# Kernel optimization log

Hardware: AMD Instinct MI355X
Metric: run time of the kernel (lower is better)

## Reference

```python
import jax, jax.numpy as jnp
import numpy as np


def _rx(state, theta, axis):
    # Apply RX(theta) to qubit at tensor axis `axis`. state: (B, 2,...,2) complex.
    half = theta * 0.5
    c = jnp.cos(half)
    s = jnp.sin(half)
    a0 = jnp.take(state, 0, axis=axis)
    a1 = jnp.take(state, 1, axis=axis)
    return jnp.stack([c * a0 - 1j * s * a1, c * a1 - 1j * s * a0], axis=axis)


def _cnot(state, w):
    # CNOT with control wire w (axis w+1), target wire w+1 (axis w+2).
    c_ax = w + 1
    s0 = jnp.take(state, 0, axis=c_ax)
    # after removing the control axis, the target axis index becomes c_ax
    s1 = jnp.flip(jnp.take(state, 1, axis=c_ax), axis=c_ax)
    return jnp.stack([s0, s1], axis=c_ax)


def _run_circuit(x, params):
    # x: (B, n) encoding angles; params: (depth, n) trainable RX angles.
    B, n = x.shape
    depth = params.shape[0]
    state = jnp.zeros((B,) + (2,) * n, jnp.complex64)
    state = state.at[(slice(None),) + (0,) * n].set(1.0 + 0.0j)
    # angle encoding: RX(x_w) on each wire
    for w in range(n):
        theta = x[:, w].reshape((B,) + (1,) * (n - 1))
        state = _rx(state, theta, w + 1)
    # variational layers: RX(param) per wire, then CNOT chain
    for d in range(depth):
        for w in range(n):
            state = _rx(state, params[d, w], w + 1)
        for w in range(n - 1):
            state = _cnot(state, w)
    probs = state.real ** 2 + state.imag ** 2  # (B, 2,...,2)
    ez = []
    for w in range(n):
        axes = tuple(a for a in range(1, n + 1) if a != w + 1)
        p = probs.sum(axes)  # (B, 2)
        ez.append(p[:, 0] - p[:, 1])  # <Z_w>
    return jnp.stack(ez, axis=1)  # (B, n)


def setup_inputs() -> dict:
    key = jax.random.key(0)
    k0, k1, k2, k3, k4 = jax.random.split(key, 5)
    seq_len, batch, input_dim = 256, 128, 64
    n_qubits, depth, hidden = 10, 2, 256
    inputs = jax.random.normal(k0, (seq_len, batch, input_dim), jnp.float32)
    mask = jax.random.randint(k1, (seq_len, batch), 0, 2).astype(jnp.int32)
    qparams = jax.random.normal(k2, (4, depth, n_qubits), jnp.float32)
    W = jax.random.normal(k3, (4, hidden, n_qubits), jnp.float32) / np.sqrt(n_qubits)
    b = jax.random.normal(k4, (4, hidden), jnp.float32) * 0.01
    return {"inputs": inputs, "mask": mask, "qparams": qparams, "W": W, "b": b}


def reference(inputs, mask, qparams, W, b):
    seq_len, batch, _ = inputs.shape
    n = qparams.shape[-1]
    hidden = W.shape[1]
    maskf = mask.astype(inputs.dtype)

    circuits4 = jax.vmap(_run_circuit, in_axes=(None, 0))  # over the 4 gates

    def step(carry, xm):
        hx, cx = carry
        x_t, m_t = xm
        q_in = jnp.concatenate([x_t, hx], axis=1)[:, :n]  # (B, n)
        z = circuits4(q_in, qparams)                      # (4, B, n)
        pre = jnp.einsum('gbn,ghn->gbh', z, W) + b[:, None, :]
        f = jax.nn.sigmoid(pre[0])
        i = jax.nn.sigmoid(pre[1])
        g = jnp.tanh(pre[2])
        o = jax.nn.sigmoid(pre[3])
        m = m_t[:, None]
        f = f * m + (1.0 - m)
        i = i * m
        g = g * m
        o = o * m + (1.0 - m)
        cx_new = f * cx + i * g
        hx_new = o * jnp.tanh(cx_new)
        return (hx_new, cx_new), hx_new

    h0 = jnp.zeros((batch, hidden), inputs.dtype)
    c0 = jnp.zeros((batch, hidden), inputs.dtype)
    (hx, cx), outputs = jax.lax.scan(jax.checkpoint(step), (h0, c0), (inputs, maskf))
    return outputs, (hx, cx)
```

## Files before the change

kernel.cpp:

```cpp
#include <hip/hip_runtime.h>

#define T_LEN 256
#define BATCH 128
#define NQ 10
#define HID 256
#define OUT_HX (T_LEN * BATCH * HID)
#define OUT_CX (OUT_HX + BATCH * HID)
#define ZSTRIDE 40
#define ZROW 44
#define TROW 65

#define KS  (-1.44269504089f)
#define KT2 (-2.88539008178f)

__global__ __launch_bounds__(256) void zker(
    const float* __restrict__ inputs,
    const float* __restrict__ qparams,
    float* __restrict__ zws)
{
  const int b   = blockIdx.x;
  const int tq  = blockIdx.y;
  const int tid = threadIdx.x;
  const int t   = tq * 64 + (tid >> 2);
  const int g   = tid & 3;

  const float sg = (g == 2) ? KT2 : KS;

  float th0[NQ], cth[NQ], sth[NQ];
#pragma unroll
  for (int k = 0; k < NQ; ++k) {
    th0[k]   = qparams[g * 2 * NQ + k];
    float t1 = qparams[g * 2 * NQ + NQ + k];
    sth[k] = __sinf(t1);
    cth[k] = __cosf(t1);
  }
  float cphi[NQ], sphi[NQ];
  const float* xp = inputs + (t * BATCH + b) * 64;
#pragma unroll
  for (int k = 0; k < NQ; ++k) {
    float ang = xp[k] + th0[k];
    sphi[k] = __sinf(ang);
    cphi[k] = __cosf(ang);
  }
  float* zout = zws + (b * T_LEN + t) * ZSTRIDE + g;
#pragma unroll
  for (int w = 0; w < NQ; ++w) {
    float vI, vZ, vY, vX; int js;
    if (w == NQ - 1) { vI = 0.f; vZ = cth[NQ-1]; vY = sth[NQ-1]; vX = 0.f; js = NQ - 2; }
    else             { vI = 1.f; vZ = 0.f; vY = 0.f; vX = 0.f; js = w; }
#pragma unroll
    for (int j = js; j >= 0; --j) {
      float nI = cth[j] * (cphi[j+1] * vZ - sphi[j+1] * vY);
      float nZ = cth[j] * vI;
      float nY = sth[j] * vX;
      float nX = -sth[j] * (sphi[j+1] * vZ + cphi[j+1] * vY);
      vI = nI; vZ = nZ; vY = nY; vX = nX;
    }
    zout[w * 4] = (vI + cphi[0] * vZ - sphi[0] * vY) * sg;
  }
}

__global__ __launch_bounds__(512) void scanker(
    const float* __restrict__ zws,
    const int*  __restrict__ mask,
    const float* __restrict__ W,
    const float* __restrict__ bias,
    float* __restrict__ out)
{
  const int b    = blockIdx.x;
  const int h0   = blockIdx.y * 64;
  const int tid  = threadIdx.x;
  const int lane = tid & 63;
  const int wavu = __builtin_amdgcn_readfirstlane(tid >> 6);

  __shared__ float zlds[T_LEN * ZROW];
  __shared__ float tlds[64 * TROW];
  __shared__ float mk[T_LEN];

  {
    const float4* zg = (const float4*)(zws + b * T_LEN * ZSTRIDE);
    for (int i = tid; i < T_LEN * 10; i += 512) {
      int t = i / 10, c4 = i - t * 10;
      *(float4*)&zlds[t * ZROW + c4 * 4] = zg[i];
    }
  }
  for (int t = tid; t < T_LEN; t += 512) mk[t] = (float)mask[t * BATCH + b];
  __syncthreads();

  float carry[8];
#pragma unroll
  for (int i = 0; i < 8; ++i) carry[i] = 0.f;

  for (int r = 0; r < 4; ++r) {
    const int t = r * 64 + lane;
    float4 z4[10];
#pragma unroll
    for (int n = 0; n < NQ; ++n) z4[n] = *(const float4*)&zlds[t * ZROW + n * 4];
    const float m = mk[t];
    const float onem = 1.f - m;

#pragma unroll
    for (int hh = 0; hh < 8; ++hh) {
      const int h = h0 + wavu * 8 + hh;
      const int wb = __builtin_amdgcn_readfirstlane(h * NQ);

      float p0 = bias[0 * HID + h] * KS;
      float p1 = bias[1 * HID + h] * KS;
      float p2 = bias[2 * HID + h] * KT2;
      float p3 = bias[3 * HID + h] * KS;
#pragma unroll
      for (int n = 0; n < NQ; ++n) {
        p0 = fmaf(z4[n].x, W[0 * HID * NQ + wb + n], p0);
        p1 = fmaf(z4[n].y, W[1 * HID * NQ + wb + n], p1);
        p2 = fmaf(z4[n].z, W[2 * HID * NQ + wb + n], p2);
        p3 = fmaf(z4[n].w, W[3 * HID * NQ + wb + n], p3);
      }
      const float uf = __builtin_amdgcn_rcpf(1.f + __builtin_amdgcn_exp2f(p0));
      const float ui = __builtin_amdgcn_rcpf(1.f + __builtin_amdgcn_exp2f(p1));
      const float ug = __builtin_amdgcn_rcpf(1.f + __builtin_amdgcn_exp2f(p2));
      const float uo = __builtin_amdgcn_rcpf(1.f + __builtin_amdgcn_exp2f(p3));

      const float fm = fmaf(m, uf, onem);
      const float gb = fmaf(2.f, ug, -1.f);
      float wt = m * ui * gb;
      const float om = fmaf(m, uo, onem);

      float a = fm, wv = wt;
#pragma unroll
      for (int d = 1; d < 64; d <<= 1) {
        float au = __shfl_up(a, d, 64);
        float wu = __shfl_up(wv, d, 64);
        const bool p = (lane >= d);
        au = p ? au : 1.f;
        wu = p ? wu : 0.f;
        wv = fmaf(a, wu, wv);
        a  = a * au;
      }
      const float ct = fmaf(a, carry[hh], wv);
      carry[hh] = __shfl(ct, 63, 64);

      const float ec = __builtin_amdgcn_exp2f(ct * KT2);
      const float tc = fmaf(2.f, __builtin_amdgcn_rcpf(1.f + ec), -1.f);
      const float hv = om * tc;

      tlds[lane * TROW + wavu * 8 + hh] = hv;

      if (r == 3 && lane == 63) {
        out[OUT_HX + b * HID + h] = hv;
        out[OUT_CX + b * HID + h] = ct;
      }
    }
    __syncthreads();
#pragma unroll
    for (int s = 0; s < 2; ++s) {
      const int q = tid + s * 512;
      const int tt = q >> 4, c = q & 15;
      float4 v;
      v.x = tlds[tt * TROW + 4 * c + 0];
      v.y = tlds[tt * TROW + 4 * c + 1];
      v.z = tlds[tt * TROW + 4 * c + 2];
      v.w = tlds[tt * TROW + 4 * c + 3];
      *(float4*)&out[(r * 64 + tt) * (BATCH * HID) + b * HID + h0 + 4 * c] = v;
    }
    __syncthreads();
  }
}

extern "C" void kernel_launch(void* const* d_in, const int* in_sizes, int n_in,
                              void* d_out, int out_size, void* d_ws, size_t ws_size,
                              hipStream_t stream)
{
  int ii = 0, im = 1, iq = 2, iw = 3, ib = 4;
  for (int i = 0; i < n_in; ++i) {
    switch (in_sizes[i]) {
      case 2097152: ii = i; break;
      case 32768:   im = i; break;
      case 80:      iq = i; break;
      case 10240:   iw = i; break;
      case 1024:    ib = i; break;
      default: break;
    }
  }
  const float* inputs  = (const float*)d_in[ii];
  const int*   mask    = (const int*)d_in[im];
  const float* qparams = (const float*)d_in[iq];
  const float* W       = (const float*)d_in[iw];
  const float* bias    = (const float*)d_in[ib];
  float*       out     = (float*)d_out;
  float*       zws     = (float*)d_ws;

  zker<<<dim3(BATCH, 4), dim3(256), 0, stream>>>(inputs, qparams, zws);
  scanker<<<dim3(BATCH, 4), dim3(512), 0, stream>>>(zws, mask, W, bias, out);
}
```

Before: 108.3 us.

## Interleave gate math with wave scans and double-buffer output staging

Changes the z workspace layout to qubit-major float4 rows so LDS loads are contiguous per timestep. Hoists the bias loads out of the time loop and precomputes the bpermute source indices. Interleaves the gate evaluation of four hidden units with the scan levels of four others, using ds_bpermute, to hide the cross-lane latency. Double-buffers the transpose staging buffer so the trailing barrier can be dropped. The cost is more live registers, which may hurt occupancy at 512 threads.

New measurement: 108.8 us. About the same (+0.5%).

```diff
diff --git a/kernel.cpp b/kernel.cpp
--- a/kernel.cpp
+++ b/kernel.cpp
@@ -6,8 +6,6 @@
 #define HID 256
 #define OUT_HX (T_LEN * BATCH * HID)
 #define OUT_CX (OUT_HX + BATCH * HID)
-#define ZSTRIDE 40
-#define ZROW 44
 #define TROW 65
 
 #define KS  (-1.44269504089f)
@@ -42,7 +40,7 @@
     sphi[k] = __sinf(ang);
     cphi[k] = __cosf(ang);
   }
-  float* zout = zws + (b * T_LEN + t) * ZSTRIDE + g;
+  float* zout = zws + (b * NQ * T_LEN + t) * 4 + g;
 #pragma unroll
   for (int w = 0; w < NQ; ++w) {
     float vI, vZ, vY, vX; int js;
@@ -56,9 +54,61 @@
       float nX = -sth[j] * (sphi[j+1] * vZ + cphi[j+1] * vY);
       vI = nI; vZ = nZ; vY = nY; vX = nX;
     }
-    zout[w * 4] = (vI + cphi[0] * vZ - sphi[0] * vY) * sg;
+    zout[w * T_LEN * 4] = (vI + cphi[0] * vZ - sphi[0] * vY) * sg;
   }
 }
+
+
+#define GATEBODY(HH)                                                     \
+  {                                                                      \
+    const int h_ = h0 + wavu * 8 + (HH);                                 \
+    const int wb_ = __builtin_amdgcn_readfirstlane(h_ * NQ);             \
+    float p0 = bsc[HH][0], p1 = bsc[HH][1], p2 = bsc[HH][2], p3 = bsc[HH][3]; \
+    _Pragma("unroll")                                                    \
+    for (int n = 0; n < NQ; ++n) {                                       \
+      p0 = fmaf(z4[n].x, W[0 * HID * NQ + wb_ + n], p0);                 \
+      p1 = fmaf(z4[n].y, W[1 * HID * NQ + wb_ + n], p1);                 \
+      p2 = fmaf(z4[n].z, W[2 * HID * NQ + wb_ + n], p2);                 \
+      p3 = fmaf(z4[n].w, W[3 * HID * NQ + wb_ + n], p3);                 \
+    }                                                                    \
+    const float uf = __builtin_amdgcn_rcpf(1.f + __builtin_amdgcn_exp2f(p0)); \
+    const float ui = __builtin_amdgcn_rcpf(1.f + __builtin_amdgcn_exp2f(p1)); \
+    const float ug = __builtin_amdgcn_rcpf(1.f + __builtin_amdgcn_exp2f(p2)); \
+    const float uo = __builtin_amdgcn_rcpf(1.f + __builtin_amdgcn_exp2f(p3)); \
+    a8[HH]  = fmaf(m, uf, onem);                                         \
+    w8[HH]  = m * ui * fmaf(2.f, ug, -1.f);                              \
+    om8[HH] = fmaf(m, uo, onem);                                         \
+  }
+
+#define BP(SRC, V) __int_as_float(__builtin_amdgcn_ds_bpermute((SRC), __float_as_int(V)))
+
+#define SCANLEV1(K, HH)                                                  \
+  {                                                                      \
+    float au = BP(srcA[K], a8[HH]);                                      \
+    float wu = BP(srcA[K], w8[HH]);                                      \
+    au = pm[K] ? au : 1.f;                                               \
+    wu = pm[K] ? wu : 0.f;                                               \
+    w8[HH] = fmaf(a8[HH], wu, w8[HH]);                                   \
+    a8[HH] = a8[HH] * au;                                                \
+  }
+
+#define SCANLEV4(K, H0, H1, H2, H3)                                      \
+  SCANLEV1(K, H0) SCANLEV1(K, H1) SCANLEV1(K, H2) SCANLEV1(K, H3)
+
+#define CPHASE(HH)                                                       \
+  {                                                                      \
+    const float ct = fmaf(a8[HH], carry[HH], w8[HH]);                    \
+    carry[HH] = __shfl(ct, 63, 64);                                      \
+    const float ec = __builtin_amdgcn_exp2f(ct * KT2);                   \
+    const float tc = fmaf(2.f, __builtin_amdgcn_rcpf(1.f + ec), -1.f);   \
+    const float hv = om8[HH] * tc;                                       \
+    tlds[p][lane * TROW + wavu * 8 + (HH)] = hv;                         \
+    if (r == 3 && lane == 63) {                                          \
+      const int h_ = h0 + wavu * 8 + (HH);                               \
+      out[OUT_HX + b * HID + h_] = hv;                                   \
+      out[OUT_CX + b * HID + h_] = ct;                                   \
+    }                                                                    \
+  }
 
 __global__ __launch_bounds__(512) void scanker(
     const float* __restrict__ zws,
@@ -73,96 +123,77 @@
   const int lane = tid & 63;
   const int wavu = __builtin_amdgcn_readfirstlane(tid >> 6);
 
-  __shared__ float zlds[T_LEN * ZROW];
-  __shared__ float tlds[64 * TROW];
-  __shared__ float mk[T_LEN];
+  __shared__ float4 zl4[NQ * T_LEN];
+  __shared__ float  tlds[2][64 * TROW];
+  __shared__ float  mk[T_LEN];
 
   {
-    const float4* zg = (const float4*)(zws + b * T_LEN * ZSTRIDE);
-    for (int i = tid; i < T_LEN * 10; i += 512) {
-      int t = i / 10, c4 = i - t * 10;
-      *(float4*)&zlds[t * ZROW + c4 * 4] = zg[i];
-    }
+    const float4* zg = (const float4*)(zws + b * NQ * T_LEN * 4);
+    for (int i = tid; i < NQ * T_LEN; i += 512) zl4[i] = zg[i];
   }
   for (int t = tid; t < T_LEN; t += 512) mk[t] = (float)mask[t * BATCH + b];
   __syncthreads();
 
+  int srcA[6]; bool pm[6];
+#pragma unroll
+  for (int k = 0; k < 6; ++k) {
+    const int d = 1 << k;
+    pm[k]   = (lane >= d);
+    srcA[k] = ((lane >= d) ? (lane - d) : lane) << 2;
+  }
+
+  float bsc[8][4];
+#pragma unroll
+  for (int hh = 0; hh < 8; ++hh) {
+    const int h = h0 + wavu * 8 + hh;
+    bsc[hh][0] = bias[0 * HID + h] * KS;
+    bsc[hh][1] = bias[1 * HID + h] * KS;
+    bsc[hh][2] = bias[2 * HID + h] * KT2;
+    bsc[hh][3] = bias[3 * HID + h] * KS;
+  }
+
   float carry[8];
 #pragma unroll
   for (int i = 0; i < 8; ++i) carry[i] = 0.f;
 
   for (int r = 0; r < 4; ++r) {
+    const int p = r & 1;
     const int t = r * 64 + lane;
-    float4 z4[10];
-#pragma unroll
-    for (int n = 0; n < NQ; ++n) z4[n] = *(const float4*)&zlds[t * ZROW + n * 4];
+    float4 z4[NQ];
+#pragma unroll
+    for (int n = 0; n < NQ; ++n) z4[n] = zl4[n * T_LEN + t];
     const float m = mk[t];
     const float onem = 1.f - m;
 
-#pragma unroll
-    for (int hh = 0; hh < 8; ++hh) {
-      const int h = h0 + wavu * 8 + hh;
-      const int wb = __builtin_amdgcn_readfirstlane(h * NQ);
-
-      float p0 = bias[0 * HID + h] * KS;
-      float p1 = bias[1 * HID + h] * KS;
-      float p2 = bias[2 * HID + h] * KT2;
-      float p3 = bias[3 * HID + h] * KS;
-#pragma unroll
-      for (int n = 0; n < NQ; ++n) {
-        p0 = fmaf(z4[n].x, W[0 * HID * NQ + wb + n], p0);
-        p1 = fmaf(z4[n].y, W[1 * HID * NQ + wb + n], p1);
-        p2 = fmaf(z4[n].z, W[2 * HID * NQ + wb + n], p2);
-        p3 = fmaf(z4[n].w, W[3 * HID * NQ + wb + n], p3);
-      }
-      const float uf = __builtin_amdgcn_rcpf(1.f + __builtin_amdgcn_exp2f(p0));
-      const float ui = __builtin_amdgcn_rcpf(1.f + __builtin_amdgcn_exp2f(p1));
-      const float ug = __builtin_amdgcn_rcpf(1.f + __builtin_amdgcn_exp2f(p2));
-      const float uo = __builtin_amdgcn_rcpf(1.f + __builtin_amdgcn_exp2f(p3));
-
-      const float fm = fmaf(m, uf, onem);
-      const float gb = fmaf(2.f, ug, -1.f);
-      float wt = m * ui * gb;
-      const float om = fmaf(m, uo, onem);
-
-      float a = fm, wv = wt;
-#pragma unroll
-      for (int d = 1; d < 64; d <<= 1) {
-        float au = __shfl_up(a, d, 64);
-        float wu = __shfl_up(wv, d, 64);
-        const bool p = (lane >= d);
-        au = p ? au : 1.f;
-        wu = p ? wu : 0.f;
-        wv = fmaf(a, wu, wv);
-        a  = a * au;
-      }
-      const float ct = fmaf(a, carry[hh], wv);
-      carry[hh] = __shfl(ct, 63, 64);
-
-      const float ec = __builtin_amdgcn_exp2f(ct * KT2);
-      const float tc = fmaf(2.f, __builtin_amdgcn_rcpf(1.f + ec), -1.f);
-      const float hv = om * tc;
-
-      tlds[lane * TROW + wavu * 8 + hh] = hv;
-
-      if (r == 3 && lane == 63) {
-        out[OUT_HX + b * HID + h] = hv;
-        out[OUT_CX + b * HID + h] = ct;
-      }
-    }
+    float a8[8], w8[8], om8[8];
+
+    GATEBODY(0) GATEBODY(1) GATEBODY(2) GATEBODY(3)
+    SCANLEV4(0, 0, 1, 2, 3) GATEBODY(4)
+    SCANLEV4(1, 0, 1, 2, 3) GATEBODY(5)
+    SCANLEV4(2, 0, 1, 2, 3) GATEBODY(6)
+    SCANLEV4(3, 0, 1, 2, 3) GATEBODY(7)
+    SCANLEV4(4, 0, 1, 2, 3)
+    SCANLEV4(5, 0, 1, 2, 3)
+    SCANLEV4(0, 4, 5, 6, 7) CPHASE(0)
+    SCANLEV4(1, 4, 5, 6, 7) CPHASE(1)
+    SCANLEV4(2, 4, 5, 6, 7) CPHASE(2)
+    SCANLEV4(3, 4, 5, 6, 7) CPHASE(3)
+    SCANLEV4(4, 4, 5, 6, 7)
+    SCANLEV4(5, 4, 5, 6, 7)
+    CPHASE(4) CPHASE(5) CPHASE(6) CPHASE(7)
+
     __syncthreads();
 #pragma unroll
     for (int s = 0; s < 2; ++s) {
       const int q = tid + s * 512;
       const int tt = q >> 4, c = q & 15;
       float4 v;
-      v.x = tlds[tt * TROW + 4 * c + 0];
-      v.y = tlds[tt * TROW + 4 * c + 1];
-      v.z = tlds[tt * TROW + 4 * c + 2];
-      v.w = tlds[tt * TROW + 4 * c + 3];
+      v.x = tlds[p][tt * TROW + 4 * c + 0];
+      v.y = tlds[p][tt * TROW + 4 * c + 1];
+      v.z = tlds[p][tt * TROW + 4 * c + 2];
+      v.w = tlds[p][tt * TROW + 4 * c + 3];
       *(float4*)&out[(r * 64 + tt) * (BATCH * HID) + b * HID + h0 + 4 * c] = v;
     }
-    __syncthreads();
   }
 }
 
```

## Restructure scan kernel: hidden units on lanes, chunked time scan across waves

Applied to the files above, without the earlier changes.

Rewrites the scan kernel so each lane owns one hidden unit with its W rows kept in registers, and each wave processes a 32-step time chunk sequentially. Chunk summaries (A, Wc) are combined through LDS, then each wave recomputes its chunk with the correct carry-in and writes outputs directly with coalesced stores across lanes. This removes the 64-lane shuffle scans, the LDS staging of z and of the output transpose, and the per-element W loads. In exchange the gate preactivations are computed twice and z rows are read from global memory as wave-uniform loads. It also adds an occupancy hint to launch bounds.

New measurement: 111.8 us. 3.2% more time.

```diff
diff --git a/kernel.cpp b/kernel.cpp
--- a/kernel.cpp
+++ b/kernel.cpp
@@ -6,9 +6,6 @@
 #define HID 256
 #define OUT_HX (T_LEN * BATCH * HID)
 #define OUT_CX (OUT_HX + BATCH * HID)
-#define ZSTRIDE 40
-#define ZROW 44
-#define TROW 65
 
 #define KS  (-1.44269504089f)
 #define KT2 (-2.88539008178f)
@@ -42,7 +39,7 @@
     sphi[k] = __sinf(ang);
     cphi[k] = __cosf(ang);
   }
-  float* zout = zws + (b * T_LEN + t) * ZSTRIDE + g;
+  float* zout = zws + (b * T_LEN + t) * 40 + g;
 #pragma unroll
   for (int w = 0; w < NQ; ++w) {
     float vI, vZ, vY, vX; int js;
@@ -60,7 +57,7 @@
   }
 }
 
-__global__ __launch_bounds__(512) void scanker(
+__global__ __launch_bounds__(512, 4) void scanker(
     const float* __restrict__ zws,
     const int*  __restrict__ mask,
     const float* __restrict__ W,
@@ -72,97 +69,95 @@
   const int tid  = threadIdx.x;
   const int lane = tid & 63;
   const int wavu = __builtin_amdgcn_readfirstlane(tid >> 6);
+  const int h    = h0 + lane;
 
-  __shared__ float zlds[T_LEN * ZROW];
-  __shared__ float tlds[64 * TROW];
   __shared__ float mk[T_LEN];
+  __shared__ float cA[8][64];
+  __shared__ float cW[8][64];
 
-  {
-    const float4* zg = (const float4*)(zws + b * T_LEN * ZSTRIDE);
-    for (int i = tid; i < T_LEN * 10; i += 512) {
-      int t = i / 10, c4 = i - t * 10;
-      *(float4*)&zlds[t * ZROW + c4 * 4] = zg[i];
-    }
+  for (int t = tid; t < T_LEN; t += 512) mk[t] = (float)mask[t * BATCH + b];
+
+  float Wf[NQ], Wi[NQ], Wg[NQ], Wo[NQ];
+#pragma unroll
+  for (int n = 0; n < NQ; ++n) {
+    Wf[n] = W[(0 * HID + h) * NQ + n];
+    Wi[n] = W[(1 * HID + h) * NQ + n];
+    Wg[n] = W[(2 * HID + h) * NQ + n];
+    Wo[n] = W[(3 * HID + h) * NQ + n];
   }
-  for (int t = tid; t < T_LEN; t += 512) mk[t] = (float)mask[t * BATCH + b];
+  const float bf = bias[0 * HID + h] * KS;
+  const float bi = bias[1 * HID + h] * KS;
+  const float bg = bias[2 * HID + h] * KT2;
+  const float bo = bias[3 * HID + h] * KS;
+
+  const float* zb = zws + b * T_LEN * 40;
   __syncthreads();
 
-  float carry[8];
+  float A = 1.f, Wc = 0.f;
+  for (int k = 0; k < 32; ++k) {
+    const int t = wavu * 32 + k;
+    const float4* zrow = (const float4*)(zb + t * 40);
+    float4 z4[NQ];
 #pragma unroll
-  for (int i = 0; i < 8; ++i) carry[i] = 0.f;
-
-  for (int r = 0; r < 4; ++r) {
-    const int t = r * 64 + lane;
-    float4 z4[10];
-#pragma unroll
-    for (int n = 0; n < NQ; ++n) z4[n] = *(const float4*)&zlds[t * ZROW + n * 4];
+    for (int n = 0; n < NQ; ++n) z4[n] = zrow[n];
     const float m = mk[t];
     const float onem = 1.f - m;
+    float p0 = bf, p1 = bi, p2 = bg;
+#pragma unroll
+    for (int n = 0; n < NQ; ++n) {
+      p0 = fmaf(z4[n].x, Wf[n], p0);
+      p1 = fmaf(z4[n].y, Wi[n], p1);
+      p2 = fmaf(z4[n].z, Wg[n], p2);
+    }
+    const float uf = __builtin_amdgcn_rcpf(1.f + __builtin_amdgcn_exp2f(p0));
+    const float ui = __builtin_amdgcn_rcpf(1.f + __builtin_amdgcn_exp2f(p1));
+    const float ug = __builtin_amdgcn_rcpf(1.f + __builtin_amdgcn_exp2f(p2));
+    const float a  = fmaf(m, uf, onem);
+    const float wt = m * ui * fmaf(2.f, ug, -1.f);
+    Wc = fmaf(a, Wc, wt);
+    A  = a * A;
+  }
+  cA[wavu][lane] = A;
+  cW[wavu][lane] = Wc;
+  __syncthreads();
 
+  float c = 0.f;
+  for (int k = 0; k < wavu; ++k)
+    c = fmaf(cA[k][lane], c, cW[k][lane]);
+
+  float hv = 0.f;
+  for (int k = 0; k < 32; ++k) {
+    const int t = wavu * 32 + k;
+    const float4* zrow = (const float4*)(zb + t * 40);
+    float4 z4[NQ];
 #pragma unroll
-    for (int hh = 0; hh < 8; ++hh) {
-      const int h = h0 + wavu * 8 + hh;
-      const int wb = __builtin_amdgcn_readfirstlane(h * NQ);
-
-      float p0 = bias[0 * HID + h] * KS;
-      float p1 = bias[1 * HID + h] * KS;
-      float p2 = bias[2 * HID + h] * KT2;
-      float p3 = bias[3 * HID + h] * KS;
+    for (int n = 0; n < NQ; ++n) z4[n] = zrow[n];
+    const float m = mk[t];
+    const float onem = 1.f - m;
+    float p0 = bf, p1 = bi, p2 = bg, p3 = bo;
 #pragma unroll
-      for (int n = 0; n < NQ; ++n) {
-        p0 = fmaf(z4[n].x, W[0 * HID * NQ + wb + n], p0);
-        p1 = fmaf(z4[n].y, W[1 * HID * NQ + wb + n], p1);
-        p2 = fmaf(z4[n].z, W[2 * HID * NQ + wb + n], p2);
-        p3 = fmaf(z4[n].w, W[3 * HID * NQ + wb + n], p3);
-      }
-      const float uf = __builtin_amdgcn_rcpf(1.f + __builtin_amdgcn_exp2f(p0));
-      const float ui = __builtin_amdgcn_rcpf(1.f + __builtin_amdgcn_exp2f(p1));
-      const float ug = __builtin_amdgcn_rcpf(1.f + __builtin_amdgcn_exp2f(p2));
-      const float uo = __builtin_amdgcn_rcpf(1.f + __builtin_amdgcn_exp2f(p3));
-
-      const float fm = fmaf(m, uf, onem);
-      const float gb = fmaf(2.f, ug, -1.f);
-      float wt = m * ui * gb;
-      const float om = fmaf(m, uo, onem);
-
-      float a = fm, wv = wt;
-#pragma unroll
-      for (int d = 1; d < 64; d <<= 1) {
-        float au = __shfl_up(a, d, 64);
-        float wu = __shfl_up(wv, d, 64);
-        const bool p = (lane >= d);
-        au = p ? au : 1.f;
-        wu = p ? wu : 0.f;
-        wv = fmaf(a, wu, wv);
-        a  = a * au;
-      }
-      const float ct = fmaf(a, carry[hh], wv);
-      carry[hh] = __shfl(ct, 63, 64);
-
-      const float ec = __builtin_amdgcn_exp2f(ct * KT2);
-      const float tc = fmaf(2.f, __builtin_amdgcn_rcpf(1.f + ec), -1.f);
-      const float hv = om * tc;
-
-      tlds[lane * TROW + wavu * 8 + hh] = hv;
-
-      if (r == 3 && lane == 63) {
-        out[OUT_HX + b * HID + h] = hv;
-        out[OUT_CX + b * HID + h] = ct;
-      }
+    for (int n = 0; n < NQ; ++n) {
+      p0 = fmaf(z4[n].x, Wf[n], p0);
+      p1 = fmaf(z4[n].y, Wi[n], p1);
+      p2 = fmaf(z4[n].z, Wg[n], p2);
+      p3 = fmaf(z4[n].w, Wo[n], p3);
     }
-    __syncthreads();
-#pragma unroll
-    for (int s = 0; s < 2; ++s) {
-      const int q = tid + s * 512;
-      const int tt = q >> 4, c = q & 15;
-      float4 v;
-      v.x = tlds[tt * TROW + 4 * c + 0];
-      v.y = tlds[tt * TROW + 4 * c + 1];
-      v.z = tlds[tt * TROW + 4 * c + 2];
-      v.w = tlds[tt * TROW + 4 * c + 3];
-      *(float4*)&out[(r * 64 + tt) * (BATCH * HID) + b * HID + h0 + 4 * c] = v;
-    }
-    __syncthreads();
+    const float uf = __builtin_amdgcn_rcpf(1.f + __builtin_amdgcn_exp2f(p0));
+    const float ui = __builtin_amdgcn_rcpf(1.f + __builtin_amdgcn_exp2f(p1));
+    const float ug = __builtin_amdgcn_rcpf(1.f + __builtin_amdgcn_exp2f(p2));
+    const float uo = __builtin_amdgcn_rcpf(1.f + __builtin_amdgcn_exp2f(p3));
+    const float a  = fmaf(m, uf, onem);
+    const float wt = m * ui * fmaf(2.f, ug, -1.f);
+    const float om = fmaf(m, uo, onem);
+    c = fmaf(a, c, wt);
+    const float ec = __builtin_amdgcn_exp2f(c * KT2);
+    const float tc = fmaf(2.f, __builtin_amdgcn_rcpf(1.f + ec), -1.f);
+    hv = om * tc;
+    out[t * (BATCH * HID) + b * HID + h] = hv;
+  }
+  if (wavu == 7) {
+    out[OUT_HX + b * HID + h] = hv;
+    out[OUT_CX + b * HID + h] = c;
   }
 }
 
```
